# Kernel tuning notes

Hardware: AMD Instinct MI355X
Metric: run time of the kernel (lower is better)

The kernel has to match this reference:

```python
import jax, jax.numpy as jnp
import numpy as np
from itertools import combinations

B, F, K, V = 1024, 39, 16, 200000  # batch, fields, embed dim, vocab
EPS = 1e-3  # tf.layers.batch_normalization default epsilon


def setup_inputs() -> dict:
    key = jax.random.key(0)
    ks = jax.random.split(key, 6)
    pairs = np.array(list(combinations(range(F), 2)), dtype=np.int32)   # [741, 2]
    trips = np.array(list(combinations(range(F), 3)), dtype=np.int32)   # [9139, 3]
    P, T = pairs.shape[0], trips.shape[0]
    return {
        "feats": jax.random.randint(ks[0], (B, F), 0, V, dtype=jnp.int32),
        "w": jax.random.normal(ks[1], (V,), dtype=jnp.float32) * 0.01,
        "v": jax.random.normal(ks[2], (V, K), dtype=jnp.float32) * 0.01,
        "b": jnp.zeros((1,), dtype=jnp.float32),
        "gamma2": jnp.ones((P,), dtype=jnp.float32),
        "beta2": jnp.zeros((P,), dtype=jnp.float32),
        "gw2": jax.random.uniform(ks[3], (P,), minval=0.599, maxval=0.601, dtype=jnp.float32),
        "gamma3": jnp.ones((T,), dtype=jnp.float32),
        "beta3": jnp.zeros((T,), dtype=jnp.float32),
        "gw3": jax.random.uniform(ks[4], (T,), minval=0.599, maxval=0.601, dtype=jnp.float32),
        "rows": jnp.asarray(pairs[:, 1]),   # second element of each pair
        "cols": jnp.asarray(pairs[:, 0]),   # first element of each pair
        "i1": jnp.asarray(trips[:, 0]),
        "i2": jnp.asarray(trips[:, 1]),
        "i3": jnp.asarray(trips[:, 2]),
    }


def _batchnorm(x, gamma, beta):
    # training-mode BN over batch axis; x: [B, P]
    m = jnp.mean(x, axis=0)
    var = jnp.mean(jnp.square(x - m), axis=0)
    return (x - m) * jax.lax.rsqrt(var + EPS) * gamma + beta


def reference(feats, w, v, b, gamma2, beta2, gw2, gamma3, beta3, gw3,
              rows, cols, i1, i2, i3):
    xw = w[feats]            # [B, F]  first-order weights
    xv = v[feats]            # [B, F, K] embeddings
    l = jnp.sum(xw, axis=1)  # linear term [B]

    # second-order: gather pair embeddings, multiply, reduce over K
    level2 = jnp.sum(xv[:, rows, :] * xv[:, cols, :], axis=-1)  # [B, P]
    level2 = _batchnorm(level2, gamma2, beta2) * gw2            # soft mask
    fm_out = jnp.sum(level2, axis=-1)                           # [B]

    # third-order: gather triple embeddings
    level3 = jnp.sum(xv[:, i1, :] * xv[:, i2, :] * xv[:, i3, :], axis=-1)  # [B, T]
    level3 = _batchnorm(level3, gamma3, beta3) * gw3
    fm_out2 = jnp.sum(level3, axis=-1)                          # [B]

    logits = l + fm_out + fm_out2 + b[0]                        # [B]
    return logits
```

## Files before the change

### kernel.cpp

```cpp
#include <hip/hip_runtime.h>
#include <hip/hip_fp16.h>
#include <math.h>

#define B_ 1024
#define F_ 39
#define K_ 16
#define P_ 741
#define T_ 9139
#define NC_ 9880
#define EPS_ 1e-3f
#define YSTR 24
#define ESTR 40
#define LS2 9920

typedef _Float16 half2v __attribute__((ext_vector_type(2)));

__device__ __forceinline__ float hdot2(unsigned a, unsigned b, float acc) {
    half2v ha = __builtin_bit_cast(half2v, a);
    half2v hb = __builtin_bit_cast(half2v, b);
#if __has_builtin(__builtin_amdgcn_fdot2)
    return __builtin_amdgcn_fdot2(ha, hb, acc, false);
#else
    return acc + (float)ha.x * (float)hb.x + (float)ha.y * (float)hb.y;
#endif
}
__device__ __forceinline__ float f16f(unsigned short h) {
    return __half2float(__builtin_bit_cast(__half, h));
}

__global__ __launch_bounds__(256) void prep_k(const int* __restrict__ rows,
                                              const int* __restrict__ cols,
                                              const int* __restrict__ i1,
                                              const int* __restrict__ i2,
                                              const int* __restrict__ i3,
                                              unsigned* __restrict__ pidx,
                                              float* __restrict__ colsum,
                                              float* __restrict__ colsumsq,
                                              float* __restrict__ Cacc) {
    int c = blockIdx.x * 256 + threadIdx.x;
    if (c >= NC_) return;
    colsum[c] = 0.f;
    colsumsq[c] = 0.f;
    if (c == 0) Cacc[0] = 0.f;
    unsigned pk;
    if (c < P_) {
        pk = (unsigned)(cols[c] * ESTR) | ((unsigned)(rows[c] * ESTR) << 11);
    } else {
        int t = c - P_;
        int a = i1[t], b = i2[t], cc = i3[t];
        int p = a * (2 * F_ - 1 - a) / 2 + (b - a - 1);
        pk = (unsigned)(p * YSTR) | ((unsigned)(cc * ESTR) << 15);
    }
    pidx[c] = pk;
}

__global__ __launch_bounds__(512) void levels_k(const int* __restrict__ feats,
                                                const float* __restrict__ v,
                                                const unsigned* __restrict__ pidx,
                                                unsigned short* __restrict__ levels) {
    int b = blockIdx.x;
    int tid = threadIdx.x;
    __shared__ int tok[F_];
    __shared__ __attribute__((aligned(16))) unsigned short emb2[F_ * ESTR];
    __shared__ __attribute__((aligned(16))) unsigned short Y2[P_ * YSTR];

    unsigned short* lrow = levels + (size_t)b * LS2;

    if (tid < F_) tok[tid] = feats[b * F_ + tid];
    __syncthreads();
    for (int idx = tid; idx < F_ * K_; idx += 512) {
        int f = idx >> 4, k = idx & 15;
        emb2[f * ESTR + k] = __builtin_bit_cast(unsigned short,
                                 __float2half(v[(size_t)tok[f] * K_ + k]));
    }
    __syncthreads();

#pragma unroll 1
    for (int p = tid; p < P_; p += 512) {
        unsigned pk = pidx[p];
        int o1 = (int)(pk & 2047u);
        int o2 = (int)((pk >> 11) & 2047u);
        uint4 ua0 = *(const uint4*)&emb2[o1];
        uint4 ua1 = *(const uint4*)&emb2[o1 + 8];
        uint4 uc0 = *(const uint4*)&emb2[o2];
        uint4 uc1 = *(const uint4*)&emb2[o2 + 8];
        float s = 0.f;
        uint4 y0, y1;
#define PKMUL(dst, a, c) {                                                    \
        half2v _a = __builtin_bit_cast(half2v, a);                            \
        half2v _c = __builtin_bit_cast(half2v, c);                            \
        half2v _y = _a * _c;                                                  \
        dst = __builtin_bit_cast(unsigned, _y);                               \
        s = hdot2(a, c, s); }
        PKMUL(y0.x, ua0.x, uc0.x); PKMUL(y0.y, ua0.y, uc0.y);
        PKMUL(y0.z, ua0.z, uc0.z); PKMUL(y0.w, ua0.w, uc0.w);
        PKMUL(y1.x, ua1.x, uc1.x); PKMUL(y1.y, ua1.y, uc1.y);
        PKMUL(y1.z, ua1.z, uc1.z); PKMUL(y1.w, ua1.w, uc1.w);
#undef PKMUL
        *(uint4*)&Y2[p * YSTR] = y0;
        *(uint4*)&Y2[p * YSTR + 8] = y1;
        lrow[p] = __builtin_bit_cast(unsigned short, __float2half(s));
    }
    __syncthreads();

#pragma unroll 3
    for (int i = 0; i < (T_ + 511) / 512; ++i) {
        int t = i * 512 + tid;
        if (t < T_) {
            unsigned pk = pidx[P_ + t];
            int yb = (int)(pk & 32767u);
            int o3 = (int)(pk >> 15);
            uint4 uy0 = *(const uint4*)&Y2[yb];
            uint4 uy1 = *(const uint4*)&Y2[yb + 8];
            uint4 ue0 = *(const uint4*)&emb2[o3];
            uint4 ue1 = *(const uint4*)&emb2[o3 + 8];
            float s = 0.f;
            s = hdot2(uy0.x, ue0.x, s); s = hdot2(uy0.y, ue0.y, s);
            s = hdot2(uy0.z, ue0.z, s); s = hdot2(uy0.w, ue0.w, s);
            s = hdot2(uy1.x, ue1.x, s); s = hdot2(uy1.y, ue1.y, s);
            s = hdot2(uy1.z, ue1.z, s); s = hdot2(uy1.w, ue1.w, s);
            lrow[P_ + t] = __builtin_bit_cast(unsigned short, __float2half(s));
        }
    }
}

__global__ __launch_bounds__(256) void stats2_k(const unsigned short* __restrict__ levels,
                                                float* __restrict__ colsum,
                                                float* __restrict__ colsumsq) {
    int col = blockIdx.x * 256 + threadIdx.x;
    if (col >= NC_) return;
    const unsigned short* p = levels + (size_t)(blockIdx.y * 16) * LS2 + col;
    float s1 = 0.f, s2 = 0.f;
#pragma unroll
    for (int r = 0; r < 16; ++r) {
        float x = f16f(p[(size_t)r * LS2]);
        s1 += x;
        s2 += x * x;
    }
    atomicAdd(&colsum[col], s1);
    atomicAdd(&colsumsq[col], s2);
}

__global__ __launch_bounds__(256) void finalize_k(const float* __restrict__ colsum,
                                                  const float* __restrict__ colsumsq,
                                                  const float* __restrict__ gamma2,
                                                  const float* __restrict__ beta2,
                                                  const float* __restrict__ gw2,
                                                  const float* __restrict__ gamma3,
                                                  const float* __restrict__ beta3,
                                                  const float* __restrict__ gw3,
                                                  float* __restrict__ scale,
                                                  float* __restrict__ Cacc) {
    int col = blockIdx.x * 256 + threadIdx.x;
    float c = 0.f;
    if (col < NC_) {
        float mean = colsum[col] * (1.0f / B_);
        float var  = colsumsq[col] * (1.0f / B_) - mean * mean;
        float inv  = 1.0f / sqrtf(var + EPS_);
        float g, be, gw;
        if (col < P_) {
            g = gamma2[col]; be = beta2[col]; gw = gw2[col];
        } else {
            int t = col - P_;
            g = gamma3[t]; be = beta3[t]; gw = gw3[t];
        }
        scale[col] = gw * g * inv;
        c = gw * (be - g * inv * mean);
    }
    __shared__ float red[256];
    red[threadIdx.x] = c;
    __syncthreads();
    for (int s = 128; s > 0; s >>= 1) {
        if (threadIdx.x < s) red[threadIdx.x] += red[threadIdx.x + s];
        __syncthreads();
    }
    if (threadIdx.x == 0) atomicAdd(Cacc, red[0]);
}

__global__ __launch_bounds__(256) void out_k(const unsigned short* __restrict__ levels,
                                             const float* __restrict__ scale,
                                             const int* __restrict__ feats,
                                             const float* __restrict__ w,
                                             const float* __restrict__ Cacc,
                                             const float* __restrict__ bias,
                                             float* __restrict__ out) {
    int b = blockIdx.x, tid = threadIdx.x;
    const uint2* lv = (const uint2*)(levels + (size_t)b * LS2);
    float acc = 0.f;
    for (int idx = tid; idx < 2470; idx += 256) {
        uint2 u = lv[idx];
        float4 sc = *(const float4*)&scale[idx * 4];
        float2 f0 = __half22float2(__builtin_bit_cast(__half2, u.x));
        float2 f1 = __half22float2(__builtin_bit_cast(__half2, u.y));
        acc += sc.x * f0.x + sc.y * f0.y + sc.z * f1.x + sc.w * f1.y;
    }
    if (tid < F_) acc += w[feats[b * F_ + tid]];
    __shared__ float red[256];
    red[tid] = acc;
    __syncthreads();
    for (int s = 128; s > 0; s >>= 1) {
        if (tid < s) red[tid] += red[tid + s];
        __syncthreads();
    }
    if (tid == 0) out[b] = red[0] + Cacc[0] + bias[0];
}

extern "C" void kernel_launch(void* const* d_in, const int* in_sizes, int n_in,
                              void* d_out, int out_size, void* d_ws, size_t ws_size,
                              hipStream_t stream) {
    const int*   feats  = (const int*)d_in[0];
    const float* w      = (const float*)d_in[1];
    const float* v      = (const float*)d_in[2];
    const float* bias   = (const float*)d_in[3];
    const float* gamma2 = (const float*)d_in[4];
    const float* beta2  = (const float*)d_in[5];
    const float* gw2    = (const float*)d_in[6];
    const float* gamma3 = (const float*)d_in[7];
    const float* beta3  = (const float*)d_in[8];
    const float* gw3    = (const float*)d_in[9];
    const int*   rows   = (const int*)d_in[10];
    const int*   cols   = (const int*)d_in[11];
    const int*   i1     = (const int*)d_in[12];
    const int*   i2     = (const int*)d_in[13];
    const int*   i3     = (const int*)d_in[14];
    float*       out    = (float*)d_out;
    float*       ws     = (float*)d_ws;

    float*          scale    = ws;
    float*          colsum   = ws + 9880;
    float*          colsumsq = ws + 19760;
    float*          Cacc     = ws + 29640;
    unsigned*       pidx     = (unsigned*)(ws + 29696);
    unsigned short* levels   = (unsigned short*)(ws + 39680);

    prep_k<<<(NC_ + 255) / 256, 256, 0, stream>>>(rows, cols, i1, i2, i3,
                                                  pidx, colsum, colsumsq, Cacc);
    levels_k<<<B_, 512, 0, stream>>>(feats, v, pidx, levels);
    stats2_k<<<dim3((NC_ + 255) / 256, B_ / 16), 256, 0, stream>>>(levels, colsum, colsumsq);
    finalize_k<<<(NC_ + 255) / 256, 256, 0, stream>>>(colsum, colsumsq,
                                                      gamma2, beta2, gw2,
                                                      gamma3, beta3, gw3, scale, Cacc);
    out_k<<<B_, 256, 0, stream>>>(levels, scale, feats, w, Cacc, bias, out);
}
```

Baseline: 126.2 us.

## Replace atomic column stats with split partial sums and prefetch pair indices

The stats kernel now writes per-split partial sums to workspace (8 splits of 128 rows) instead of issuing atomicAdds from 64 row-blocks. The finalize kernel reduces those partials, so the zeroing in prep_k is no longer needed. levels_k prefetches all of its packed pidx indices into registers before the shared-memory setup, and out_k reads 8 halves per load instead of 4. The trade-off is fewer blocks in the stats kernel (lower parallelism) and higher register pressure from holding 18 prefetched indices.

```diff
diff --git a/kernel.cpp b/kernel.cpp
--- a/kernel.cpp
+++ b/kernel.cpp
@@ -12,6 +12,7 @@
 #define YSTR 24
 #define ESTR 40
 #define LS2 9920
+#define NSPLIT 8
 
 typedef _Float16 half2v __attribute__((ext_vector_type(2)));
 
@@ -34,13 +35,9 @@
                                               const int* __restrict__ i2,
                                               const int* __restrict__ i3,
                                               unsigned* __restrict__ pidx,
-                                              float* __restrict__ colsum,
-                                              float* __restrict__ colsumsq,
                                               float* __restrict__ Cacc) {
     int c = blockIdx.x * 256 + threadIdx.x;
     if (c >= NC_) return;
-    colsum[c] = 0.f;
-    colsumsq[c] = 0.f;
     if (c == 0) Cacc[0] = 0.f;
     unsigned pk;
     if (c < P_) {
@@ -66,6 +63,15 @@
 
     unsigned short* lrow = levels + (size_t)b * LS2;
 
+    unsigned pk_p0 = (tid < P_) ? pidx[tid] : 0u;
+    unsigned pk_p1 = (tid + 512 < P_) ? pidx[tid + 512] : 0u;
+    unsigned pkt[18];
+#pragma unroll
+    for (int i = 0; i < 18; ++i) {
+        int t = i * 512 + tid;
+        pkt[i] = (t < T_) ? pidx[P_ + t] : 0u;
+    }
+
     if (tid < F_) tok[tid] = feats[b * F_ + tid];
     __syncthreads();
     for (int idx = tid; idx < F_ * K_; idx += 512) {
@@ -76,38 +82,41 @@
     __syncthreads();
 
 #pragma unroll 1
-    for (int p = tid; p < P_; p += 512) {
-        unsigned pk = pidx[p];
-        int o1 = (int)(pk & 2047u);
-        int o2 = (int)((pk >> 11) & 2047u);
-        uint4 ua0 = *(const uint4*)&emb2[o1];
-        uint4 ua1 = *(const uint4*)&emb2[o1 + 8];
-        uint4 uc0 = *(const uint4*)&emb2[o2];
-        uint4 uc1 = *(const uint4*)&emb2[o2 + 8];
-        float s = 0.f;
-        uint4 y0, y1;
+    for (int pp = 0; pp < 2; ++pp) {
+        int p = pp * 512 + tid;
+        if (p < P_) {
+            unsigned pk = pp == 0 ? pk_p0 : pk_p1;
+            int o1 = (int)(pk & 2047u);
+            int o2 = (int)((pk >> 11) & 2047u);
+            uint4 ua0 = *(const uint4*)&emb2[o1];
+            uint4 ua1 = *(const uint4*)&emb2[o1 + 8];
+            uint4 uc0 = *(const uint4*)&emb2[o2];
+            uint4 uc1 = *(const uint4*)&emb2[o2 + 8];
+            float s = 0.f;
+            uint4 y0, y1;
 #define PKMUL(dst, a, c) {                                                    \
-        half2v _a = __builtin_bit_cast(half2v, a);                            \
-        half2v _c = __builtin_bit_cast(half2v, c);                            \
-        half2v _y = _a * _c;                                                  \
-        dst = __builtin_bit_cast(unsigned, _y);                               \
-        s = hdot2(a, c, s); }
-        PKMUL(y0.x, ua0.x, uc0.x); PKMUL(y0.y, ua0.y, uc0.y);
-        PKMUL(y0.z, ua0.z, uc0.z); PKMUL(y0.w, ua0.w, uc0.w);
-        PKMUL(y1.x, ua1.x, uc1.x); PKMUL(y1.y, ua1.y, uc1.y);
-        PKMUL(y1.z, ua1.z, uc1.z); PKMUL(y1.w, ua1.w, uc1.w);
+            half2v _a = __builtin_bit_cast(half2v, a);                        \
+            half2v _c = __builtin_bit_cast(half2v, c);                        \
+            half2v _y = _a * _c;                                              \
+            dst = __builtin_bit_cast(unsigned, _y);                           \
+            s = hdot2(a, c, s); }
+            PKMUL(y0.x, ua0.x, uc0.x); PKMUL(y0.y, ua0.y, uc0.y);
+            PKMUL(y0.z, ua0.z, uc0.z); PKMUL(y0.w, ua0.w, uc0.w);
+            PKMUL(y1.x, ua1.x, uc1.x); PKMUL(y1.y, ua1.y, uc1.y);
+            PKMUL(y1.z, ua1.z, uc1.z); PKMUL(y1.w, ua1.w, uc1.w);
 #undef PKMUL
-        *(uint4*)&Y2[p * YSTR] = y0;
-        *(uint4*)&Y2[p * YSTR + 8] = y1;
-        lrow[p] = __builtin_bit_cast(unsigned short, __float2half(s));
+            *(uint4*)&Y2[p * YSTR] = y0;
+            *(uint4*)&Y2[p * YSTR + 8] = y1;
+            lrow[p] = __builtin_bit_cast(unsigned short, __float2half(s));
+        }
     }
     __syncthreads();
 
 #pragma unroll 3
-    for (int i = 0; i < (T_ + 511) / 512; ++i) {
+    for (int i = 0; i < 18; ++i) {
         int t = i * 512 + tid;
         if (t < T_) {
-            unsigned pk = pidx[P_ + t];
+            unsigned pk = pkt[i];
             int yb = (int)(pk & 32767u);
             int o3 = (int)(pk >> 15);
             uint4 uy0 = *(const uint4*)&Y2[yb];
@@ -118,31 +127,39 @@
             s = hdot2(uy0.x, ue0.x, s); s = hdot2(uy0.y, ue0.y, s);
             s = hdot2(uy0.z, ue0.z, s); s = hdot2(uy0.w, ue0.w, s);
             s = hdot2(uy1.x, ue1.x, s); s = hdot2(uy1.y, ue1.y, s);
-            s = hdot2(uy1.z, ue1.z, s); s = hdot2(uy1.w, ue1.w, s);
+            s = hdot2(uy1.z, ue1.z, s);
+            s = hdot2(uy1.w, ue1.w, s);
             lrow[P_ + t] = __builtin_bit_cast(unsigned short, __float2half(s));
         }
     }
 }
 
 __global__ __launch_bounds__(256) void stats2_k(const unsigned short* __restrict__ levels,
-                                                float* __restrict__ colsum,
-                                                float* __restrict__ colsumsq) {
+                                                float* __restrict__ psum,
+                                                float* __restrict__ psumsq) {
     int col = blockIdx.x * 256 + threadIdx.x;
     if (col >= NC_) return;
-    const unsigned short* p = levels + (size_t)(blockIdx.y * 16) * LS2 + col;
-    float s1 = 0.f, s2 = 0.f;
-#pragma unroll
-    for (int r = 0; r < 16; ++r) {
-        float x = f16f(p[(size_t)r * LS2]);
-        s1 += x;
-        s2 += x * x;
-    }
-    atomicAdd(&colsum[col], s1);
-    atomicAdd(&colsumsq[col], s2);
-}
-
-__global__ __launch_bounds__(256) void finalize_k(const float* __restrict__ colsum,
-                                                  const float* __restrict__ colsumsq,
+    int sy = blockIdx.y;
+    const unsigned short* p = levels + (size_t)(sy * (B_ / NSPLIT)) * LS2 + col;
+    float a0 = 0.f, a1 = 0.f, a2 = 0.f, a3 = 0.f;
+    float q0 = 0.f, q1 = 0.f, q2 = 0.f, q3 = 0.f;
+#pragma unroll 4
+    for (int r = 0; r < B_ / NSPLIT; r += 4) {
+        float x0 = f16f(p[(size_t)(r + 0) * LS2]);
+        float x1 = f16f(p[(size_t)(r + 1) * LS2]);
+        float x2 = f16f(p[(size_t)(r + 2) * LS2]);
+        float x3 = f16f(p[(size_t)(r + 3) * LS2]);
+        a0 += x0; q0 += x0 * x0;
+        a1 += x1; q1 += x1 * x1;
+        a2 += x2; q2 += x2 * x2;
+        a3 += x3; q3 += x3 * x3;
+    }
+    psum[sy * NC_ + col]   = (a0 + a1) + (a2 + a3);
+    psumsq[sy * NC_ + col] = (q0 + q1) + (q2 + q3);
+}
+
+__global__ __launch_bounds__(256) void finalize_k(const float* __restrict__ psum,
+                                                  const float* __restrict__ psumsq,
                                                   const float* __restrict__ gamma2,
                                                   const float* __restrict__ beta2,
                                                   const float* __restrict__ gw2,
@@ -154,8 +171,14 @@
     int col = blockIdx.x * 256 + threadIdx.x;
     float c = 0.f;
     if (col < NC_) {
-        float mean = colsum[col] * (1.0f / B_);
-        float var  = colsumsq[col] * (1.0f / B_) - mean * mean;
+        float s1 = 0.f, s2 = 0.f;
+#pragma unroll
+        for (int sy = 0; sy < NSPLIT; ++sy) {
+            s1 += psum[sy * NC_ + col];
+            s2 += psumsq[sy * NC_ + col];
+        }
+        float mean = s1 * (1.0f / B_);
+        float var  = s2 * (1.0f / B_) - mean * mean;
         float inv  = 1.0f / sqrtf(var + EPS_);
         float g, be, gw;
         if (col < P_) {
@@ -185,14 +208,18 @@
                                              const float* __restrict__ bias,
                                              float* __restrict__ out) {
     int b = blockIdx.x, tid = threadIdx.x;
-    const uint2* lv = (const uint2*)(levels + (size_t)b * LS2);
+    const uint4* lv = (const uint4*)(levels + (size_t)b * LS2);
     float acc = 0.f;
-    for (int idx = tid; idx < 2470; idx += 256) {
-        uint2 u = lv[idx];
-        float4 sc = *(const float4*)&scale[idx * 4];
+    for (int idx = tid; idx < 1235; idx += 256) {
+        uint4 u = lv[idx];
+        float4 sa = *(const float4*)&scale[idx * 8];
+        float4 sb = *(const float4*)&scale[idx * 8 + 4];
         float2 f0 = __half22float2(__builtin_bit_cast(__half2, u.x));
         float2 f1 = __half22float2(__builtin_bit_cast(__half2, u.y));
-        acc += sc.x * f0.x + sc.y * f0.y + sc.z * f1.x + sc.w * f1.y;
+        float2 f2 = __half22float2(__builtin_bit_cast(__half2, u.z));
+        float2 f3 = __half22float2(__builtin_bit_cast(__half2, u.w));
+        acc += sa.x * f0.x + sa.y * f0.y + sa.z * f1.x + sa.w * f1.y;
+        acc += sb.x * f2.x + sb.y * f2.y + sb.z * f3.x + sb.w * f3.y;
     }
     if (tid < F_) acc += w[feats[b * F_ + tid]];
     __shared__ float red[256];
@@ -227,17 +254,16 @@
     float*       ws     = (float*)d_ws;
 
     float*          scale    = ws;
-    float*          colsum   = ws + 9880;
-    float*          colsumsq = ws + 19760;
-    float*          Cacc     = ws + 29640;
-    unsigned*       pidx     = (unsigned*)(ws + 29696);
-    unsigned short* levels   = (unsigned short*)(ws + 39680);
-
-    prep_k<<<(NC_ + 255) / 256, 256, 0, stream>>>(rows, cols, i1, i2, i3,
-                                                  pidx, colsum, colsumsq, Cacc);
+    float*          psum     = ws + 9880;
+    float*          psumsq   = ws + 88920;
+    float*          Cacc     = ws + 167960;
+    unsigned*       pidx     = (unsigned*)(ws + 168064);
+    unsigned short* levels   = (unsigned short*)(ws + 177984);
+
+    prep_k<<<(NC_ + 255) / 256, 256, 0, stream>>>(rows, cols, i1, i2, i3, pidx, Cacc);
     levels_k<<<B_, 512, 0, stream>>>(feats, v, pidx, levels);
-    stats2_k<<<dim3((NC_ + 255) / 256, B_ / 16), 256, 0, stream>>>(levels, colsum, colsumsq);
-    finalize_k<<<(NC_ + 255) / 256, 256, 0, stream>>>(colsum, colsumsq,
+    stats2_k<<<dim3((NC_ + 255) / 256, NSPLIT), 256, 0, stream>>>(levels, psum, psumsq);
+    finalize_k<<<(NC_ + 255) / 256, 256, 0, stream>>>(psum, psumsq,
                                                       gamma2, beta2, gw2,
                                                       gamma3, beta3, gw3, scale, Cacc);
     out_k<<<B_, 256, 0, stream>>>(levels, scale, feats, w, Cacc, bias, out);
```

Measured after the change: 123.3 us. 2.3% less time.
